# Kernel optimization log

Hardware: AMD Instinct MI355X
Metric: run time of the kernel (lower is better)

Reference implementation:

```python
import jax, jax.numpy as jnp
import numpy as np

B, T, D = 4, 8192, 1024
C = 8.0


def setup_inputs() -> dict:
    key = jax.random.key(0)
    k1, k2, k3 = jax.random.split(key, 3)
    init_std = D ** (-0.5)
    x = jax.random.normal(k1, (B, T, D), dtype=jnp.float32)
    W_in = jax.random.truncated_normal(k2, -3.0, 3.0, (D, D), dtype=jnp.float32) * init_std
    W_gate = jax.random.truncated_normal(k3, -3.0, 3.0, (D, D), dtype=jnp.float32) * init_std
    b_in = jnp.zeros((D,), dtype=jnp.float32)
    b_gate = jnp.zeros((D,), dtype=jnp.float32)
    forget_lambda = jnp.linspace(-4.323, -9.0, D, dtype=jnp.float32)
    return {"x": x, "W_in": W_in, "b_in": b_in, "W_gate": W_gate,
            "b_gate": b_gate, "forget_lambda": forget_lambda}


def _combine(c1, c2):
    # linear recurrence h_t = a_t * h_{t-1} + b_t  (associative composition)
    a1, b1 = c1
    a2, b2 = c2
    return a1 * a2, a2 * b1 + b2


def reference(x, W_in, b_in, W_gate, b_gate, forget_lambda):
    # x: [B, T, D]
    input_gate = x @ W_in.T + b_in          # [B, T, D]
    recurrence_gate = x @ W_gate.T + b_gate  # [B, T, D]
    alpha = jnp.exp(-C * jax.nn.softplus(forget_lambda) * jax.nn.sigmoid(recurrence_gate))
    beta = jnp.sqrt(1.0 - alpha ** 2 + 1e-6)
    xbeta = beta * jax.nn.sigmoid(input_gate) * x
    # parallel scan of h_t = alpha_t * h_{t-1} + xbeta_t along sequence axis
    _, h = jax.lax.associative_scan(_combine, (alpha, xbeta), axis=1)
    return h
```

## Files before the change

### kernel.cpp

```cpp
#include <hip/hip_runtime.h>

typedef unsigned short u16;
typedef __attribute__((ext_vector_type(8))) short short8;
typedef __attribute__((ext_vector_type(4))) float f32x4;

#define T_SEQ 8192
#define DDIM 1024
#define BB 4
#define MM (BB * T_SEQ)
#define NC 128
#define CHUNK (T_SEQ / NC)
#define CHAINS (BB * DDIM)

__device__ __forceinline__ float bf_lo(unsigned p) {
    union { unsigned u; float f; } v; v.u = p << 16; return v.f;
}
__device__ __forceinline__ float bf_hi(unsigned p) {
    union { unsigned u; float f; } v; v.u = p & 0xffff0000u; return v.f;
}
__device__ __forceinline__ float bf_u16(u16 p) {
    union { unsigned u; float f; } v; v.u = ((unsigned)p) << 16; return v.f;
}
__device__ __forceinline__ u16 f2bf(float f) {
    union { unsigned u; float f; } v; v.f = f;
    unsigned r = v.u + 0x7fffu + ((v.u >> 16) & 1u);
    return (u16)(r >> 16);
}
__device__ __forceinline__ float sigm(float z) {
    return __builtin_amdgcn_rcpf(1.0f + __expf(-z));
}
__device__ __forceinline__ void gld16(const u16* g, u16* l) {
    __builtin_amdgcn_global_load_lds((const __attribute__((address_space(1))) void*)g,
                                     (__attribute__((address_space(3))) void*)l, 16, 0, 0);
}

#define N4X (MM * DDIM / 4)
#define N4W (DDIM * DDIM / 4)
__global__ __launch_bounds__(256) void cvt_all(const float* __restrict__ x,
                                               const float* __restrict__ Wi,
                                               const float* __restrict__ Wg,
                                               u16* __restrict__ Xb,
                                               u16* __restrict__ Wib,
                                               u16* __restrict__ Wgb) {
    int i = blockIdx.x * 256 + threadIdx.x;
    const float* src; u16* dst; int j;
    if (i < N4X)            { src = x;  dst = Xb;  j = i; }
    else if (i < N4X + N4W) { src = Wi; dst = Wib; j = i - N4X; }
    else                    { src = Wg; dst = Wgb; j = i - N4X - N4W; }
    float4 v = ((const float4*)src)[j];
    ushort4 o;
    o.x = f2bf(v.x); o.y = f2bf(v.y); o.z = f2bf(v.z); o.w = f2bf(v.w);
    ((ushort4*)dst)[j] = o;
}

__global__ __launch_bounds__(512, 4)
void gemm_fused(const u16* __restrict__ X, const u16* __restrict__ Wi,
                const u16* __restrict__ Wg, const float* __restrict__ b_in,
                const float* __restrict__ b_gate, const float* __restrict__ lam,
                u16* __restrict__ Sg, u16* __restrict__ XBg) {
    const int b = blockIdx.x;
    const int xcd = b & 7;
    const int r = b >> 3;
    const int n_tile = r & 7;
    const int m_tile = xcd * 32 + (r >> 3);
    const int tN0 = n_tile * 128;
    const int tM0 = m_tile * 128;

    const int tid = threadIdx.x;
    const int lane = tid & 63;
    const int w = tid >> 6;
    const int gate = w >> 2;
    const int wq = w & 3;
    const int wm = wq >> 1, wn = wq & 1;

    __shared__ u16 lA[128 * 32];
    __shared__ u16 lBi[128 * 32];
    __shared__ u16 lBg[128 * 32];
    __shared__ u16 ex[4 * 4 * 4 * 64];

    const u16* gA  = X  + (size_t)(tM0 + (tid >> 2)) * DDIM + (tid & 3) * 8;
    const u16* gBi = Wi + (size_t)(tN0 + (tid >> 2)) * DDIM + (tid & 3) * 8;
    const u16* gBg = Wg + (size_t)(tN0 + (tid >> 2)) * DDIM + (tid & 3) * 8;
    u16* lA0  = &lA[tid * 8];
    u16* lBi0 = &lBi[tid * 8];
    u16* lBg0 = &lBg[tid * 8];

    f32x4 acc[4][4] = {};
    const int lm = lane & 15;
    const int q8 = (lane >> 4) * 8;
    const u16* lB = gate ? lBg : lBi;

    for (int k0 = 0; k0 < DDIM; k0 += 32) {
        __syncthreads();
        gld16(gA, lA0);
        gld16(gBi, lBi0);
        gld16(gBg, lBg0);
        gA += 32; gBi += 32; gBg += 32;
        __syncthreads();

        short8 af[4], bfr[4];
#pragma unroll
        for (int i = 0; i < 4; i++)
            af[i] = *(const short8*)&lA[(wm * 64 + i * 16 + lm) * 32 + q8];
#pragma unroll
        for (int j = 0; j < 4; j++)
            bfr[j] = *(const short8*)&lB[(wn * 64 + j * 16 + lm) * 32 + q8];
#pragma unroll
        for (int i = 0; i < 4; i++)
#pragma unroll
            for (int j = 0; j < 4; j++)
                acc[i][j] = __builtin_amdgcn_mfma_f32_16x16x32_bf16(af[i], bfr[j], acc[i][j], 0, 0, 0);
    }

    const int r0 = (lane >> 4) << 2;
    const int cb = lane & 15;
#pragma unroll
    for (int j = 0; j < 4; j++) {
        __syncthreads();
        const int colg = tN0 + wn * 64 + j * 16 + cb;
        if (gate) {
            const float bj = b_gate[colg];
            const float nsp = -8.0f * log1pf(__expf(lam[colg]));
#pragma unroll
            for (int i = 0; i < 4; i++) {
                const int rowb = tM0 + wm * 64 + i * 16 + r0;
#pragma unroll
                for (int rr = 0; rr < 4; rr++) {
                    float s = nsp * sigm(acc[i][j][rr] + bj);
                    u16 sb = f2bf(s);
                    Sg[(size_t)(rowb + rr) * DDIM + colg] = sb;
                    ex[((wq * 4 + i) * 4 + rr) * 64 + lane] = sb;
                }
            }
        }
        __syncthreads();
        if (!gate) {
            const float bj = b_in[colg];
#pragma unroll
            for (int i = 0; i < 4; i++) {
                const int rowb = tM0 + wm * 64 + i * 16 + r0;
#pragma unroll
                for (int rr = 0; rr < 4; rr++) {
                    float s = bf_u16(ex[((wq * 4 + i) * 4 + rr) * 64 + lane]);
                    float a2 = __expf(2.0f * s);
                    float be = sqrtf(1.0f - a2 + 1e-6f);
                    float p = sigm(acc[i][j][rr] + bj);
                    float xv = bf_u16(X[(size_t)(rowb + rr) * DDIM + colg]);
                    XBg[(size_t)(rowb + rr) * DDIM + colg] = f2bf(be * p * xv);
                }
            }
        }
    }
}

__global__ __launch_bounds__(256)
void scan_pass1(const u16* __restrict__ S, const u16* __restrict__ XB,
                float* __restrict__ AggA, float* __restrict__ AggB) {
    const int c = blockIdx.x, dblk = blockIdx.y, bq = blockIdx.z;
    const int d0 = dblk * 512 + threadIdx.x * 2;
    size_t base = ((size_t)(bq * T_SEQ + c * CHUNK)) * DDIM + d0;

    float A0 = 1.0f, B0 = 0.0f, A1 = 1.0f, B1 = 0.0f;
#pragma unroll 8
    for (int t = 0; t < CHUNK; t++) {
        unsigned sp = *(const unsigned*)(S + base);
        unsigned xp = *(const unsigned*)(XB + base);
        float a0 = __expf(bf_lo(sp));
        float a1 = __expf(bf_hi(sp));
        B0 = fmaf(a0, B0, bf_lo(xp)); A0 *= a0;
        B1 = fmaf(a1, B1, bf_hi(xp)); A1 *= a1;
        base += DDIM;
    }
    const int chain = bq * DDIM + d0;
    float2 av; av.x = A0; av.y = A1;
    float2 bv; bv.x = B0; bv.y = B1;
    *(float2*)(AggA + (size_t)c * CHAINS + chain) = av;
    *(float2*)(AggB + (size_t)c * CHAINS + chain) = bv;
}

__global__ __launch_bounds__(256)
void scan_pass2(const float* __restrict__ AggA, const float* __restrict__ AggB,
                float* __restrict__ H0) {
    const int chain = blockIdx.x * 256 + threadIdx.x;
    float p = 0.0f;
#pragma unroll 8
    for (int c = 0; c < NC; c++) {
        H0[(size_t)c * CHAINS + chain] = p;
        p = AggA[(size_t)c * CHAINS + chain] * p + AggB[(size_t)c * CHAINS + chain];
    }
}

__global__ __launch_bounds__(256)
void scan_pass3(const u16* __restrict__ S, const u16* __restrict__ XB,
                const float* __restrict__ H0, float* __restrict__ out) {
    const int c = blockIdx.x, dblk = blockIdx.y, bq = blockIdx.z;
    const int d0 = dblk * 512 + threadIdx.x * 2;
    size_t base = ((size_t)(bq * T_SEQ + c * CHUNK)) * DDIM + d0;
    const int chain = bq * DDIM + d0;

    float2 h = *(const float2*)(H0 + (size_t)c * CHAINS + chain);
#pragma unroll 8
    for (int t = 0; t < CHUNK; t++) {
        unsigned sp = *(const unsigned*)(S + base);
        unsigned xp = *(const unsigned*)(XB + base);
        float a0 = __expf(bf_lo(sp));
        float a1 = __expf(bf_hi(sp));
        h.x = fmaf(a0, h.x, bf_lo(xp));
        h.y = fmaf(a1, h.y, bf_hi(xp));
        *(float2*)(out + base) = h;
        base += DDIM;
    }
}

extern "C" void kernel_launch(void* const* d_in, const int* in_sizes, int n_in,
                              void* d_out, int out_size, void* d_ws, size_t ws_size,
                              hipStream_t stream) {
    const float* x   = (const float*)d_in[0];
    const float* Win = (const float*)d_in[1];
    const float* bin = (const float*)d_in[2];
    const float* Wg  = (const float*)d_in[3];
    const float* bg  = (const float*)d_in[4];
    const float* lam = (const float*)d_in[5];
    float* out = (float*)d_out;

    char* w = (char*)d_ws;
    u16* Wi_bf  = (u16*)(w);
    u16* Wg_bf  = (u16*)(w + (size_t)(2) * 1024 * 1024);
    u16* Sg     = (u16*)(w + (size_t)(4) * 1024 * 1024);
    u16* XBg    = (u16*)(w + (size_t)(68) * 1024 * 1024);
    float* AggA = (float*)(w + (size_t)(132) * 1024 * 1024);
    float* AggB = (float*)(w + (size_t)(134) * 1024 * 1024);
    float* H0   = (float*)(w + (size_t)(136) * 1024 * 1024);

    u16* Xbf = (u16*)d_out;

    cvt_all<<<dim3((N4X + 2 * N4W) / 256), dim3(256), 0, stream>>>(
        x, Win, Wg, Xbf, Wi_bf, Wg_bf);

    gemm_fused<<<dim3((DDIM / 128) * (MM / 128)), dim3(512), 0, stream>>>(
        Xbf, Wi_bf, Wg_bf, bin, bg, lam, Sg, XBg);

    scan_pass1<<<dim3(NC, 2, BB), dim3(256), 0, stream>>>(Sg, XBg, AggA, AggB);
    scan_pass2<<<dim3(CHAINS / 256), dim3(256), 0, stream>>>(AggA, AggB, H0);
    scan_pass3<<<dim3(NC, 2, BB), dim3(256), 0, stream>>>(Sg, XBg, H0, out);
}
```

Before: 509.4 us.

## Double-buffer GEMM LDS with swizzled layout and larger 256-row M tiles

Rewrites the fused dual GEMM main loop to use a 128 KB double-buffered LDS region. Global-to-LDS loads for the next K-step are issued while MFMAs run on the current one, with explicit waitcnt, barriers and setprio scheduling. The M tile doubles to 256 rows so each wave does 8x4 MFMA tiles, and the LDS layout is XOR-swizzled to reduce bank conflicts. This costs occupancy (launch bounds drop to 2 blocks per CU) and adds hand-tuned synchronisation that is fragile to get right.

```diff
diff --git a/kernel.cpp b/kernel.cpp
--- a/kernel.cpp
+++ b/kernel.cpp
@@ -11,6 +11,7 @@
 #define NC 128
 #define CHUNK (T_SEQ / NC)
 #define CHAINS (BB * DDIM)
+#define NT 16
 
 __device__ __forceinline__ float bf_lo(unsigned p) {
     union { unsigned u; float f; } v; v.u = p << 16; return v.f;
@@ -53,97 +54,148 @@
     ((ushort4*)dst)[j] = o;
 }
 
-__global__ __launch_bounds__(512, 4)
+
+#define MFMA_ROW(i_, av)                                                              \
+    acc[i_][0] = __builtin_amdgcn_mfma_f32_16x16x32_bf16(av, b0, acc[i_][0], 0, 0, 0); \
+    acc[i_][1] = __builtin_amdgcn_mfma_f32_16x16x32_bf16(av, b1, acc[i_][1], 0, 0, 0); \
+    acc[i_][2] = __builtin_amdgcn_mfma_f32_16x16x32_bf16(av, b2, acc[i_][2], 0, 0, 0); \
+    acc[i_][3] = __builtin_amdgcn_mfma_f32_16x16x32_bf16(av, b3, acc[i_][3], 0, 0, 0);
+
+#define MFMA_Q(ib) MFMA_ROW((ib)+0, a0) MFMA_ROW((ib)+1, a1) MFMA_ROW((ib)+2, a2) MFMA_ROW((ib)+3, a3)
+
+#define PH_TAIL(IB)                                          \
+    __builtin_amdgcn_s_barrier();                            \
+    asm volatile("s_waitcnt lgkmcnt(0)" ::: "memory");       \
+    __builtin_amdgcn_sched_barrier(0);                       \
+    __builtin_amdgcn_s_setprio(1);                           \
+    MFMA_Q(IB)                                               \
+    __builtin_amdgcn_s_setprio(0);                           \
+    __builtin_amdgcn_s_barrier();                            \
+    __builtin_amdgcn_sched_barrier(0);
+
+#define STA(buf, kh, rb, t_) gld16(gA + (size_t)(t_)*64 + (kh)*32 + (size_t)(rb)*128*DDIM, \
+                                   &lds[(((buf)*2 + (kh))*1024 + (rb)*512 + tid)*8])
+#define STB(buf, kh, hf, t_) gld16(((hf) ? gBg : gBi) + (size_t)(t_)*64 + (kh)*32,          \
+                                   &lds[32768 + (((buf)*2 + (kh))*1024 + (hf)*512 + tid)*8])
+
+#define LDA(kk, i) (*(const short8*)&lds[((cur*2 + (kk))*256 + arow0 + (i)*16)*32 + aoff])
+#define LDB(kk, j) (*(const short8*)&lds[32768 + ((cur*2 + (kk))*256 + brow0 + (j)*16)*32 + aoff])
+
+__global__ __launch_bounds__(512, 2)
 void gemm_fused(const u16* __restrict__ X, const u16* __restrict__ Wi,
                 const u16* __restrict__ Wg, const float* __restrict__ b_in,
                 const float* __restrict__ b_gate, const float* __restrict__ lam,
                 u16* __restrict__ Sg, u16* __restrict__ XBg) {
-    const int b = blockIdx.x;
-    const int xcd = b & 7;
-    const int r = b >> 3;
+    const int bid = blockIdx.x;
+    const int xcd = bid & 7;
+    const int r = bid >> 3;
     const int n_tile = r & 7;
-    const int m_tile = xcd * 32 + (r >> 3);
+    const int m_tile = xcd * 16 + (r >> 3);
     const int tN0 = n_tile * 128;
-    const int tM0 = m_tile * 128;
+    const int tM0 = m_tile * 256;
 
     const int tid = threadIdx.x;
     const int lane = tid & 63;
     const int w = tid >> 6;
-    const int gate = w >> 2;
-    const int wq = w & 3;
-    const int wm = wq >> 1, wn = wq & 1;
-
-    __shared__ u16 lA[128 * 32];
-    __shared__ u16 lBi[128 * 32];
-    __shared__ u16 lBg[128 * 32];
-    __shared__ u16 ex[4 * 4 * 4 * 64];
-
-    const u16* gA  = X  + (size_t)(tM0 + (tid >> 2)) * DDIM + (tid & 3) * 8;
-    const u16* gBi = Wi + (size_t)(tN0 + (tid >> 2)) * DDIM + (tid & 3) * 8;
-    const u16* gBg = Wg + (size_t)(tN0 + (tid >> 2)) * DDIM + (tid & 3) * 8;
-    u16* lA0  = &lA[tid * 8];
-    u16* lBi0 = &lBi[tid * 8];
-    u16* lBg0 = &lBg[tid * 8];
-
-    f32x4 acc[4][4] = {};
+    const int wm = w >> 2;
+    const int wn = w & 3;
+    const int gate = wn >> 1;
+    const int wn_sub = wn & 1;
+
+    __shared__ u16 lds[65536];
+
+    const int srow = tid >> 2;
+    const int c8log = (tid & 3) ^ ((tid >> 3) & 3);
+    const u16* gA  = X  + (size_t)(tM0 + srow) * DDIM + c8log * 8;
+    const u16* gBi = Wi + (size_t)(tN0 + srow) * DDIM + c8log * 8;
+    const u16* gBg = Wg + (size_t)(tN0 + srow) * DDIM + c8log * 8;
+
     const int lm = lane & 15;
-    const int q8 = (lane >> 4) * 8;
-    const u16* lB = gate ? lBg : lBi;
-
-    for (int k0 = 0; k0 < DDIM; k0 += 32) {
-        __syncthreads();
-        gld16(gA, lA0);
-        gld16(gBi, lBi0);
-        gld16(gBg, lBg0);
-        gA += 32; gBi += 32; gBg += 32;
-        __syncthreads();
-
-        short8 af[4], bfr[4];
-#pragma unroll
-        for (int i = 0; i < 4; i++)
-            af[i] = *(const short8*)&lA[(wm * 64 + i * 16 + lm) * 32 + q8];
-#pragma unroll
-        for (int j = 0; j < 4; j++)
-            bfr[j] = *(const short8*)&lB[(wn * 64 + j * 16 + lm) * 32 + q8];
-#pragma unroll
-        for (int i = 0; i < 4; i++)
-#pragma unroll
-            for (int j = 0; j < 4; j++)
-                acc[i][j] = __builtin_amdgcn_mfma_f32_16x16x32_bf16(af[i], bfr[j], acc[i][j], 0, 0, 0);
-    }
-
+    const int aoff = (((lane >> 4) ^ ((lm >> 1) & 3))) * 8;
+    const int arow0 = wm * 128 + lm;
+    const int brow0 = gate * 128 + wn_sub * 64 + lm;
+
+    f32x4 acc[8][4] = {};
+    short8 a0, a1, a2, a3, b0, b1, b2, b3;
+
+    STA(0, 0, 0, 0); STA(0, 0, 1, 0); STB(0, 0, 0, 0); STB(0, 0, 1, 0);
+    STA(0, 1, 0, 0); STA(0, 1, 1, 0); STB(0, 1, 0, 0); STB(0, 1, 1, 0);
+    asm volatile("s_waitcnt vmcnt(4)" ::: "memory");
+    __builtin_amdgcn_s_barrier();
+    __builtin_amdgcn_sched_barrier(0);
+
+    for (int t = 0; t < NT - 1; ++t) {
+        const int cur = t & 1, nb = cur ^ 1, tn = t + 1;
+        b0 = LDB(0, 0); b1 = LDB(0, 1); b2 = LDB(0, 2); b3 = LDB(0, 3);
+        a0 = LDA(0, 0); a1 = LDA(0, 1); a2 = LDA(0, 2); a3 = LDA(0, 3);
+        STA(nb, 0, 0, tn); STA(nb, 0, 1, tn);
+        PH_TAIL(0)
+        a0 = LDA(0, 4); a1 = LDA(0, 5); a2 = LDA(0, 6); a3 = LDA(0, 7);
+        STB(nb, 0, 0, tn); STB(nb, 0, 1, tn);
+        asm volatile("s_waitcnt vmcnt(4)" ::: "memory");
+        PH_TAIL(4)
+        b0 = LDB(1, 0); b1 = LDB(1, 1); b2 = LDB(1, 2); b3 = LDB(1, 3);
+        a0 = LDA(1, 0); a1 = LDA(1, 1); a2 = LDA(1, 2); a3 = LDA(1, 3);
+        STA(nb, 1, 0, tn); STA(nb, 1, 1, tn);
+        PH_TAIL(0)
+        a0 = LDA(1, 4); a1 = LDA(1, 5); a2 = LDA(1, 6); a3 = LDA(1, 7);
+        STB(nb, 1, 0, tn); STB(nb, 1, 1, tn);
+        asm volatile("s_waitcnt vmcnt(4)" ::: "memory");
+        PH_TAIL(4)
+    }
+    {
+        const int cur = (NT - 1) & 1;
+        b0 = LDB(0, 0); b1 = LDB(0, 1); b2 = LDB(0, 2); b3 = LDB(0, 3);
+        a0 = LDA(0, 0); a1 = LDA(0, 1); a2 = LDA(0, 2); a3 = LDA(0, 3);
+        PH_TAIL(0)
+        a0 = LDA(0, 4); a1 = LDA(0, 5); a2 = LDA(0, 6); a3 = LDA(0, 7);
+        asm volatile("s_waitcnt vmcnt(0)" ::: "memory");
+        PH_TAIL(4)
+        b0 = LDB(1, 0); b1 = LDB(1, 1); b2 = LDB(1, 2); b3 = LDB(1, 3);
+        a0 = LDA(1, 0); a1 = LDA(1, 1); a2 = LDA(1, 2); a3 = LDA(1, 3);
+        PH_TAIL(0)
+        a0 = LDA(1, 4); a1 = LDA(1, 5); a2 = LDA(1, 6); a3 = LDA(1, 7);
+        PH_TAIL(4)
+    }
+
+    const int pair = wm * 2 + wn_sub;
     const int r0 = (lane >> 4) << 2;
     const int cb = lane & 15;
-#pragma unroll
-    for (int j = 0; j < 4; j++) {
-        __syncthreads();
-        const int colg = tN0 + wn * 64 + j * 16 + cb;
-        if (gate) {
+    if (gate) {
+#pragma unroll
+        for (int j = 0; j < 4; ++j) {
+            const int colg = tN0 + wn_sub * 64 + j * 16 + cb;
             const float bj = b_gate[colg];
             const float nsp = -8.0f * log1pf(__expf(lam[colg]));
 #pragma unroll
-            for (int i = 0; i < 4; i++) {
-                const int rowb = tM0 + wm * 64 + i * 16 + r0;
-#pragma unroll
-                for (int rr = 0; rr < 4; rr++) {
+            for (int i = 0; i < 8; ++i) {
+                const int rowb = tM0 + wm * 128 + i * 16 + r0;
+#pragma unroll
+                for (int rr = 0; rr < 4; ++rr) {
                     float s = nsp * sigm(acc[i][j][rr] + bj);
                     u16 sb = f2bf(s);
                     Sg[(size_t)(rowb + rr) * DDIM + colg] = sb;
-                    ex[((wq * 4 + i) * 4 + rr) * 64 + lane] = sb;
+                    lds[((pair * 8 + i) * 16 + j * 4 + rr) * 64 + lane] = sb;
                 }
             }
         }
-        __syncthreads();
-        if (!gate) {
+    }
+    asm volatile("s_waitcnt lgkmcnt(0)" ::: "memory");
+    __builtin_amdgcn_s_barrier();
+    __builtin_amdgcn_sched_barrier(0);
+    if (!gate) {
+#pragma unroll
+        for (int j = 0; j < 4; ++j) {
+            const int colg = tN0 + wn_sub * 64 + j * 16 + cb;
             const float bj = b_in[colg];
 #pragma unroll
-            for (int i = 0; i < 4; i++) {
-                const int rowb = tM0 + wm * 64 + i * 16 + r0;
-#pragma unroll
-                for (int rr = 0; rr < 4; rr++) {
-                    float s = bf_u16(ex[((wq * 4 + i) * 4 + rr) * 64 + lane]);
-                    float a2 = __expf(2.0f * s);
-                    float be = sqrtf(1.0f - a2 + 1e-6f);
+            for (int i = 0; i < 8; ++i) {
+                const int rowb = tM0 + wm * 128 + i * 16 + r0;
+#pragma unroll
+                for (int rr = 0; rr < 4; ++rr) {
+                    float s = bf_u16(lds[((pair * 8 + i) * 16 + j * 4 + rr) * 64 + lane]);
+                    float a2v = __expf(2.0f * s);
+                    float be = sqrtf(1.0f - a2v + 1e-6f);
                     float p = sigm(acc[i][j][rr] + bj);
                     float xv = bf_u16(X[(size_t)(rowb + rr) * DDIM + colg]);
                     XBg[(size_t)(rowb + rr) * DDIM + colg] = f2bf(be * p * xv);
@@ -237,7 +289,7 @@
     cvt_all<<<dim3((N4X + 2 * N4W) / 256), dim3(256), 0, stream>>>(
         x, Win, Wg, Xbf, Wi_bf, Wg_bf);
 
-    gemm_fused<<<dim3((DDIM / 128) * (MM / 128)), dim3(512), 0, stream>>>(
+    gemm_fused<<<dim3((DDIM / 128) * (MM / 256)), dim3(512), 0, stream>>>(
         Xbf, Wi_bf, Wg_bf, bin, bg, lam, Sg, XBg);
 
     scan_pass1<<<dim3(NC, 2, BB), dim3(256), 0, stream>>>(Sg, XBg, AggA, AggB);
```

New measurement: 521.1 us. 2.3% more time.
